# Performance work log

Hardware: AMD Instinct MI355X
Metric: run time of the kernel (lower is better)

## Reference

```python
import jax, jax.numpy as jnp
import numpy as np

B, E, DIM, RANK, K, P, H, W, FREQ = 16, 4, 64, 32, 2, 8, 128, 128, 64
NOISE_STD = 1.0 / E


def conv1x1(x, w):
    # x: [b,c,h,w], w: [o,c]
    return jnp.einsum('bchw,oc->bohw', x, w)


def dwconv(x, w, pad):
    # depthwise conv, w: [c,1,kh,kw]
    c = x.shape[1]
    return jax.lax.conv_general_dilated(
        x, w, (1, 1), [(pad, pad), (pad, pad)],
        dimension_numbers=('NCHW', 'OIHW', 'NCHW'), feature_group_count=c)


def patchify(x):
    b, c, h, w = x.shape
    return x.reshape(b, c, h // P, P, w // P, P).transpose(0, 1, 2, 4, 3, 5)


def unpatchify(x):
    b, c, hb, wb, p1, p2 = x.shape
    return x.transpose(0, 1, 2, 4, 3, 5).reshape(b, c, hb * p1, wb * p2)


def chan_layernorm(x, w, b):
    # WithBias LayerNorm over channel dim (to_3d puts c last)
    mu = x.mean(axis=1, keepdims=True)
    var = ((x - mu) ** 2).mean(axis=1, keepdims=True)
    return (x - mu) / jnp.sqrt(var + 1e-5) * w[None, :, None, None] + b[None, :, None, None]


def fft_attention(x, qw, qdw, kvw, kvdw, lnw, lnb, pow_, pob):
    q = dwconv(conv1x1(x, qw), qdw, 1)
    kv = dwconv(conv1x1(x, kvw), kvdw, 3)
    k, v = jnp.split(kv, 2, axis=1)
    qf = jnp.fft.rfft2(patchify(q))
    kf = jnp.fft.rfft2(patchify(k))
    out = jnp.fft.irfft2(qf * kf, s=(P, P))
    out = unpatchify(out)
    out = chan_layernorm(out, lnw, lnb)
    out = out * v
    return conv1x1(out, pow_) + pob[None, :, None, None]


def expert(p0, p1, p2, qw, qdw, kvw, kvdw, lnw, lnb, pow_, pob, x, shared):
    # ModExpert.process (feat_extract with depth>1 recomputes the same value)
    xr = conv1x1(x, p0)
    att = fft_attention(xr, qw, qdw, kvw, kvdw, lnw, lnb, pow_, pob)
    g = jax.nn.silu(conv1x1(shared, p1))
    return conv1x1(att * g, p2) + x


def setup_inputs() -> dict:
    key = jax.random.key(0)
    ks = jax.random.split(key, 20)
    s = 0.05
    return {
        'x': jax.random.normal(ks[0], (B, DIM, H, W), jnp.float32),
        'shared': jax.random.normal(ks[1], (B, DIM, H, W), jnp.float32),
        'freq_emb': jax.random.normal(ks[2], (B, FREQ), jnp.float32),
        'noise': jax.random.normal(ks[3], (B, E), jnp.float32),
        'gate_w': jax.random.normal(ks[4], (E, DIM), jnp.float32) * s,
        'freq_gate_w': jax.random.normal(ks[5], (E, FREQ), jnp.float32) * s,
        'p0': jax.random.normal(ks[6], (E, RANK, DIM), jnp.float32) * s,
        'p1': jax.random.normal(ks[7], (E, RANK, DIM), jnp.float32) * s,
        'p2': jax.random.normal(ks[8], (E, DIM, RANK), jnp.float32) * s,
        'q_w': jax.random.normal(ks[9], (E, RANK, RANK), jnp.float32) * s,
        'q_dw': jax.random.normal(ks[10], (E, RANK, 1, 3, 3), jnp.float32) * s,
        'kv_w': jax.random.normal(ks[11], (E, 2 * RANK, RANK), jnp.float32) * s,
        'kv_dw': jax.random.normal(ks[12], (E, 2 * RANK, 1, 7, 7), jnp.float32) * s,
        'ln_w': jnp.ones((E, RANK), jnp.float32),
        'ln_b': jnp.zeros((E, RANK), jnp.float32),
        'po_w': jax.random.normal(ks[13], (E, RANK, RANK), jnp.float32) * s,
        'po_b': jnp.zeros((E, RANK), jnp.float32),
    }


def reference(x, shared, freq_emb, noise, gate_w, freq_gate_w, p0, p1, p2,
              q_w, q_dw, kv_w, kv_dw, ln_w, ln_b, po_w, po_b):
    # RoutingFunction (eval mode: aux_loss = 0, noise still added)
    pooled = x.mean(axis=(2, 3))                       # [B, DIM]
    logits = pooled @ gate_w.T + freq_emb @ freq_gate_w.T  # [B, E]
    noisy = logits + noise * NOISE_STD
    scores = jax.nn.softmax(noisy, axis=-1)
    vals, idx = jax.lax.top_k(scores, K)
    gates = jnp.zeros_like(scores).at[jnp.arange(B)[:, None], idx].set(vals)
    # Dense expert evaluation; gated combine == SparseDispatcher dispatch/combine
    outs = jax.vmap(expert, in_axes=(0,) * 11 + (None, None))(
        p0, p1, p2, q_w, q_dw, kv_w, kv_dw, ln_w, ln_b, po_w, po_b, x, shared)
    return jnp.einsum('be,ebchw->bchw', gates, outs)
```

## Files before the change

### kernel.cpp

```cpp
#include <hip/hip_runtime.h>
#include <hip/hip_bf16.h>

#define BATCH 16
#define DIM 64
#define RANK 32
#define H 128
#define W 128
#define HW (H*W)
#define NSLOT 32

static __device__ __forceinline__ float bu2f(unsigned short u) {
    return __uint_as_float(((unsigned)u) << 16);
}
static __device__ __forceinline__ unsigned short f2bu(float f) {
    union { __hip_bfloat16 h; unsigned short u; } cv;
    cv.h = __float2bfloat16(f);
    return cv.u;
}
static __device__ __forceinline__ float ulo(unsigned int w) { return __uint_as_float(w << 16); }
static __device__ __forceinline__ float uhi(unsigned int w) { return __uint_as_float(w & 0xffff0000u); }

__global__ __launch_bounds__(256) void k_pool(const float* __restrict__ x,
                                              float* __restrict__ pooled) {
    int bc = blockIdx.x;
    const float4* p = (const float4*)(x + (size_t)bc * HW);
    float s = 0.f;
    for (int i = threadIdx.x; i < HW / 4; i += 256) {
        float4 v = p[i];
        s += v.x + v.y + v.z + v.w;
    }
#pragma unroll
    for (int off = 32; off > 0; off >>= 1) s += __shfl_down(s, off);
    __shared__ float red[4];
    if ((threadIdx.x & 63) == 0) red[threadIdx.x >> 6] = s;
    __syncthreads();
    if (threadIdx.x == 0)
        pooled[bc] = (red[0] + red[1] + red[2] + red[3]) * (1.f / HW);
}

__global__ __launch_bounds__(64) void k_gate(const float* __restrict__ pooled,
                                             const float* __restrict__ freq_emb,
                                             const float* __restrict__ noise,
                                             const float* __restrict__ gate_w,
                                             const float* __restrict__ fgw,
                                             int* __restrict__ slot_e,
                                             float* __restrict__ slot_g,
                                             float* __restrict__ gsum) {
    int b = threadIdx.x;
    if (b >= BATCH) return;
    float lg[4];
    for (int e = 0; e < 4; e++) {
        float s = 0.f;
        for (int c = 0; c < 64; c++) s += pooled[b * 64 + c] * gate_w[e * 64 + c];
        for (int c = 0; c < 64; c++) s += freq_emb[b * 64 + c] * fgw[e * 64 + c];
        s += noise[b * 4 + e] * 0.25f;
        lg[e] = s;
    }
    float m = fmaxf(fmaxf(lg[0], lg[1]), fmaxf(lg[2], lg[3]));
    float sc[4], Z = 0.f;
    for (int e = 0; e < 4; e++) { sc[e] = expf(lg[e] - m); Z += sc[e]; }
    for (int e = 0; e < 4; e++) sc[e] /= Z;
    int i0 = 0;
    for (int e = 1; e < 4; e++) if (sc[e] > sc[i0]) i0 = e;
    int i1 = -1;
    for (int e = 0; e < 4; e++) {
        if (e == i0) continue;
        if (i1 < 0 || sc[e] > sc[i1]) i1 = e;
    }
    slot_e[2 * b] = i0;     slot_g[2 * b] = sc[i0];
    slot_e[2 * b + 1] = i1; slot_g[2 * b + 1] = sc[i1];
    gsum[b] = sc[i0] + sc[i1];
}

__global__ __launch_bounds__(256) void k_weff(const float* __restrict__ q_w,
                                              const float* __restrict__ kv_w,
                                              const float* __restrict__ p0,
                                              float* __restrict__ weff) {
    int t = blockIdx.x * 256 + threadIdx.x;
    if (t >= 4 * 96 * 64) return;
    int c = t & 63;
    int j = (t >> 6) % 96;
    int e = t / (96 * 64);
    const float* p0p = p0 + (size_t)e * RANK * DIM;
    float s = 0.f;
    if (j < 32) {
        const float* qp = q_w + (e * 32 + j) * 32;
        for (int r = 0; r < 32; r++) s += qp[r] * p0p[r * DIM + c];
    } else {
        const float* kp = kv_w + (e * 64 + (j - 32)) * 32;
        for (int r = 0; r < 32; r++) s += kp[r] * p0p[r * DIM + c];
    }
    weff[(e * 64 + c) * 96 + j] = s;
}

__global__ __launch_bounds__(256) void k_xpose(const float* __restrict__ po_w,
                                               const float* __restrict__ p1,
                                               float* __restrict__ powf,
                                               float* __restrict__ p1f) {
    int t = blockIdx.x * 256 + threadIdx.x;
    if (t < 4096) {
        int e = t >> 10, oc = (t >> 5) & 31, c = t & 31;
        powf[(e * 32 + c) * 32 + oc] = po_w[t];
    }
    int e = t >> 11, j = (t >> 6) & 31, c = t & 63;
    p1f[(e * 64 + c) * 32 + j] = p1[t];
}

__global__ __launch_bounds__(256) void k_qkvpre(const float* __restrict__ x,
                                                const float* __restrict__ weff,
                                                const int* __restrict__ slot_e,
                                                unsigned short* __restrict__ qkvpre) {
    int t = blockIdx.x;
    int jg = t % 3;
    int tile = (t / 3) & 15;
    int slot = t / 48;
    int b = slot >> 1;
    int e = slot_e[slot];
    const float* wp = weff + e * 96 * 64 + jg * 32;
    int p0 = tile * 1024 + threadIdx.x * 4;
    const float* xb = x + (size_t)b * DIM * HW + p0;
    float a0[32], a1[32], a2[32], a3[32];
#pragma unroll
    for (int j = 0; j < 32; j++) { a0[j] = 0.f; a1[j] = 0.f; a2[j] = 0.f; a3[j] = 0.f; }
    for (int c = 0; c < DIM; c++) {
        float4 xv = *(const float4*)(xb + (size_t)c * HW);
        const float* wr = wp + c * 96;
#pragma unroll
        for (int j = 0; j < 32; j++) {
            float wv = wr[j];
            a0[j] += wv * xv.x; a1[j] += wv * xv.y; a2[j] += wv * xv.z; a3[j] += wv * xv.w;
        }
    }
    unsigned short* op = qkvpre + ((size_t)slot * 96 + jg * 32) * HW + p0;
#pragma unroll
    for (int j = 0; j < 32; j++) {
        ushort4 o4;
        o4.x = f2bu(a0[j]); o4.y = f2bu(a1[j]); o4.z = f2bu(a2[j]); o4.w = f2bu(a3[j]);
        *(ushort4*)(op + (size_t)j * HW) = o4;
    }
}

__global__ __launch_bounds__(256) void k_dw(const unsigned short* __restrict__ qkvpre,
                                            const float* __restrict__ q_dw,
                                            const float* __restrict__ kv_dw,
                                            const int* __restrict__ slot_e,
                                            unsigned short* __restrict__ qkv) {
    __shared__ unsigned short S[38][144];
    int t = blockIdx.x;
    int tile = t & 3;
    int c = (t >> 2) % 96;
    int slot = t / (96 * 4);
    int e = slot_e[slot];
    const unsigned short* in = qkvpre + ((size_t)slot * 96 + c) * HW;
    int y0 = tile * 32 - 3;

    float wk[49];
    if (c < 32) {
        const float* wp = q_dw + (e * 32 + c) * 9;
#pragma unroll
        for (int i = 0; i < 9; i++) wk[i] = wp[i];
    } else {
        const float* wp = kv_dw + (e * 64 + (c - 32)) * 49;
#pragma unroll
        for (int i = 0; i < 49; i++) wk[i] = wp[i];
    }

    for (int i = threadIdx.x; i < 38 * 16; i += 256) {
        int r = i >> 4;
        int xc = (i & 15) << 3;
        int yy = y0 + r;
        uint4 v = make_uint4(0u, 0u, 0u, 0u);
        if (yy >= 0 && yy < H) v = *(const uint4*)(in + (size_t)yy * W + xc);
        *(uint4*)&S[r][8 + xc] = v;
    }
    for (int i = threadIdx.x; i < 38 * 2; i += 256) {
        int r = i >> 1;
        *(uint4*)&S[r][(i & 1) ? 136 : 0] = make_uint4(0u, 0u, 0u, 0u);
    }
    __syncthreads();

    int tx = (threadIdx.x & 31) * 4;
    int ty0 = (threadIdx.x >> 5) * 4;
    float acc[4][4];
#pragma unroll
    for (int a_ = 0; a_ < 4; a_++)
#pragma unroll
        for (int b_ = 0; b_ < 4; b_++) acc[a_][b_] = 0.f;

    if (c < 32) {
#pragma unroll
        for (int rr = 0; rr < 6; rr++) {
            int srow = ty0 + 2 + rr;
            float px[12];
            uint2 w0 = *(const uint2*)&S[srow][4 + tx];
            uint2 w1 = *(const uint2*)&S[srow][8 + tx];
            uint2 w2 = *(const uint2*)&S[srow][12 + tx];
            px[0] = ulo(w0.x); px[1] = uhi(w0.x); px[2] = ulo(w0.y); px[3] = uhi(w0.y);
            px[4] = ulo(w1.x); px[5] = uhi(w1.x); px[6] = ulo(w1.y); px[7] = uhi(w1.y);
            px[8] = ulo(w2.x); px[9] = uhi(w2.x); px[10] = ulo(w2.y); px[11] = uhi(w2.y);
#pragma unroll
            for (int ly = 0; ly < 4; ly++) {
                int ky = rr - ly;
                if (ky < 0 || ky > 2) continue;
#pragma unroll
                for (int kx = 0; kx < 3; kx++) {
                    float wv = wk[ky * 3 + kx];
#pragma unroll
                    for (int j = 0; j < 4; j++) acc[ly][j] += wv * px[j + kx + 3];
                }
            }
        }
    } else {
#pragma unroll
        for (int rr = 0; rr < 10; rr++) {
            int srow = ty0 + rr;
            float px[12];
            uint2 w0 = *(const uint2*)&S[srow][4 + tx];
            uint2 w1 = *(const uint2*)&S[srow][8 + tx];
            uint2 w2 = *(const uint2*)&S[srow][12 + tx];
            px[0] = ulo(w0.x); px[1] = uhi(w0.x); px[2] = ulo(w0.y); px[3] = uhi(w0.y);
            px[4] = ulo(w1.x); px[5] = uhi(w1.x); px[6] = ulo(w1.y); px[7] = uhi(w1.y);
            px[8] = ulo(w2.x); px[9] = uhi(w2.x); px[10] = ulo(w2.y); px[11] = uhi(w2.y);
#pragma unroll
            for (int ly = 0; ly < 4; ly++) {
                int ky = rr - ly;
                if (ky < 0 || ky > 6) continue;
#pragma unroll
                for (int kx = 0; kx < 7; kx++) {
                    float wv = wk[ky * 7 + kx];
#pragma unroll
                    for (int j = 0; j < 4; j++) acc[ly][j] += wv * px[j + kx + 1];
                }
            }
        }
    }

    unsigned short* op = qkv + ((size_t)slot * 96 + c) * HW;
    int ybase = tile * 32 + ty0;
#pragma unroll
    for (int ly = 0; ly < 4; ly++) {
        ushort4 o4;
        o4.x = f2bu(acc[ly][0]); o4.y = f2bu(acc[ly][1]);
        o4.z = f2bu(acc[ly][2]); o4.w = f2bu(acc[ly][3]);
        *(ushort4*)(op + (size_t)(ybase + ly) * W + tx) = o4;
    }
}

__global__ __launch_bounds__(256) void k_circ(const unsigned short* __restrict__ qkv,
                                              unsigned short* __restrict__ obuf) {
    __shared__ float Qs[32][68];
    __shared__ float Kp[32][68];
    int u = threadIdx.x >> 3;
    int i = threadIdx.x & 7;
    int U = blockIdx.x * 32 + u;
    int patch = U & 255;
    int c = (U >> 8) & 31;
    int slot = U >> 13;
    int py = patch >> 4, px = patch & 15;
    size_t rowbase = ((size_t)slot * 96 + c) * HW + (py * 8 + i) * W + px * 8;
    uint4 qu = *(const uint4*)(qkv + rowbase);
    uint4 ku = *(const uint4*)(qkv + rowbase + (size_t)32 * HW);
    float qr[8], kr[8];
    qr[0] = ulo(qu.x); qr[1] = uhi(qu.x); qr[2] = ulo(qu.y); qr[3] = uhi(qu.y);
    qr[4] = ulo(qu.z); qr[5] = uhi(qu.z); qr[6] = ulo(qu.w); qr[7] = uhi(qu.w);
    kr[0] = ulo(ku.x); kr[1] = uhi(ku.x); kr[2] = ulo(ku.y); kr[3] = uhi(ku.y);
    kr[4] = ulo(ku.z); kr[5] = uhi(ku.z); kr[6] = ulo(ku.w); kr[7] = uhi(ku.w);
    *(float4*)&Qs[u][i * 8] = *(float4*)&qr[0];
    *(float4*)&Qs[u][i * 8 + 4] = *(float4*)&qr[4];
    *(float4*)&Kp[u][i * 8] = *(float4*)&kr[0];
    *(float4*)&Kp[u][i * 8 + 4] = *(float4*)&kr[4];
    __syncthreads();
    float acc[8];
#pragma unroll
    for (int j = 0; j < 8; j++) acc[j] = 0.f;
#pragma unroll
    for (int mi = 0; mi < 8; mi++) {
        int r = (i - mi) & 7;
        float qv[8], ka[4], kb[4];
        *(float4*)&qv[0] = *(const float4*)&Qs[u][mi * 8];
        *(float4*)&qv[4] = *(const float4*)&Qs[u][mi * 8 + 4];
        *(float4*)&ka[0] = *(const float4*)&Kp[u][r * 8];
        *(float4*)&kb[0] = *(const float4*)&Kp[u][r * 8 + 4];
#pragma unroll
        for (int j = 0; j < 8; j++) {
            float s = acc[j];
#pragma unroll
            for (int t = 0; t < 4; t++) {
                s += ka[t] * qv[(j - t) & 7];
                s += kb[t] * qv[(j - 4 - t) & 7];
            }
            acc[j] = s;
        }
    }
    size_t obase = ((size_t)slot * 32 + c) * HW + (py * 8 + i) * W + px * 8;
    uint4 ov;
    ov.x = (unsigned)f2bu(acc[0]) | ((unsigned)f2bu(acc[1]) << 16);
    ov.y = (unsigned)f2bu(acc[2]) | ((unsigned)f2bu(acc[3]) << 16);
    ov.z = (unsigned)f2bu(acc[4]) | ((unsigned)f2bu(acc[5]) << 16);
    ov.w = (unsigned)f2bu(acc[6]) | ((unsigned)f2bu(acc[7]) << 16);
    *(uint4*)(obuf + obase) = ov;
}

__global__ __launch_bounds__(256) void k_att(const unsigned short* __restrict__ obuf,
                                             const unsigned short* __restrict__ qkv,
                                             const float* __restrict__ shr,
                                             const int* __restrict__ slot_e,
                                             const float* __restrict__ slot_g,
                                             const float* __restrict__ powf,
                                             const float* __restrict__ po_b,
                                             const float* __restrict__ ln_w,
                                             const float* __restrict__ ln_b,
                                             const float* __restrict__ p1f,
                                             unsigned short* __restrict__ attg) {
    int slot = blockIdx.x >> 6;
    int p = ((blockIdx.x & 63) << 8) + threadIdx.x;
    int b = slot >> 1;
    int e = slot_e[slot];
    float g = slot_g[slot];

    const unsigned short* op = obuf + (size_t)slot * 32 * HW + p;
    float o[32];
#pragma unroll
    for (int c = 0; c < 32; c++) o[c] = bu2f(op[(size_t)c * HW]);
    float mu = 0.f;
#pragma unroll
    for (int c = 0; c < 32; c++) mu += o[c];
    mu *= (1.f / 32.f);
    float var = 0.f;
#pragma unroll
    for (int c = 0; c < 32; c++) { float d = o[c] - mu; var += d * d; }
    float rinv = rsqrtf(var * (1.f / 32.f) + 1e-5f);
    const float* powp = powf + e * 1024;
    const float* lnwp = ln_w + e * 32;
    const float* lnbp = ln_b + e * 32;
    const float* pobp = po_b + e * 32;
    const unsigned short* vp = qkv + ((size_t)slot * 96 + 64) * HW + p;
    float att[32];
#pragma unroll
    for (int j = 0; j < 32; j++) att[j] = pobp[j];
    for (int c = 0; c < 32; c++) {
        float uu = ((o[c] - mu) * rinv * lnwp[c] + lnbp[c]) * bu2f(vp[(size_t)c * HW]);
        const float* pr = powp + c * 32;
#pragma unroll
        for (int j = 0; j < 32; j++) att[j] += pr[j] * uu;
    }

    float t[32];
#pragma unroll
    for (int j = 0; j < 32; j++) t[j] = 0.f;
    const float* shp = shr + (size_t)b * 64 * HW + p;
    const float* p1p = p1f + e * 2048;
    for (int c = 0; c < 64; c++) {
        float sv = shp[(size_t)c * HW];
        const float* pr = p1p + c * 32;
#pragma unroll
        for (int j = 0; j < 32; j++) t[j] += pr[j] * sv;
    }

    unsigned short* ap = attg + ((size_t)slot * HW + p) * 32;
    unsigned int wbuf[16];
#pragma unroll
    for (int jj = 0; jj < 16; jj++) {
        float t0 = t[2 * jj], t1 = t[2 * jj + 1];
        float a0 = g * att[2 * jj] * t0 * __builtin_amdgcn_rcpf(1.f + __expf(-t0));
        float a1 = g * att[2 * jj + 1] * t1 * __builtin_amdgcn_rcpf(1.f + __expf(-t1));
        wbuf[jj] = (unsigned)f2bu(a0) | ((unsigned)f2bu(a1) << 16);
    }
#pragma unroll
    for (int q = 0; q < 4; q++)
        *(uint4*)(ap + q * 8) = *(uint4*)&wbuf[q * 4];
}

__global__ __launch_bounds__(256) void k_comb(const unsigned short* __restrict__ attg,
                                              const float* __restrict__ x,
                                              const int* __restrict__ slot_e,
                                              const float* __restrict__ gsum,
                                              const float* __restrict__ p2,
                                              float* __restrict__ out) {
    int t = blockIdx.x;
    int oh = t & 1;
    int tile = (t >> 1) & 63;
    int b = t >> 7;
    int p = (tile << 8) + threadIdx.x;

    const unsigned short* a0p = attg + ((size_t)(2 * b) * HW + p) * 32;
    const unsigned short* a1p = attg + ((size_t)(2 * b + 1) * HW + p) * 32;
    float a0[32], a1[32];
#pragma unroll
    for (int q = 0; q < 4; q++) {
        uint4 u0 = *(const uint4*)(a0p + q * 8);
        uint4 u1 = *(const uint4*)(a1p + q * 8);
        a0[q * 8 + 0] = ulo(u0.x); a0[q * 8 + 1] = uhi(u0.x);
        a0[q * 8 + 2] = ulo(u0.y); a0[q * 8 + 3] = uhi(u0.y);
        a0[q * 8 + 4] = ulo(u0.z); a0[q * 8 + 5] = uhi(u0.z);
        a0[q * 8 + 6] = ulo(u0.w); a0[q * 8 + 7] = uhi(u0.w);
        a1[q * 8 + 0] = ulo(u1.x); a1[q * 8 + 1] = uhi(u1.x);
        a1[q * 8 + 2] = ulo(u1.y); a1[q * 8 + 3] = uhi(u1.y);
        a1[q * 8 + 4] = ulo(u1.z); a1[q * 8 + 5] = uhi(u1.z);
        a1[q * 8 + 6] = ulo(u1.w); a1[q * 8 + 7] = uhi(u1.w);
    }
    int e0 = slot_e[2 * b], e1 = slot_e[2 * b + 1];
    float gs = gsum[b];
    const float* p2a = p2 + e0 * 2048 + oh * 1024;
    const float* p2b = p2 + e1 * 2048 + oh * 1024;
    const float* xp = x + ((size_t)b * 64 + oh * 32) * HW + p;
    float* oa = out + ((size_t)b * 64 + oh * 32) * HW + p;
    for (int oc = 0; oc < 32; oc++) {
        const float* pa = p2a + oc * 32;
        const float* pb = p2b + oc * 32;
        float sa = 0.f, sb = 0.f;
#pragma unroll
        for (int j = 0; j < 32; j++) {
            sa += pa[j] * a0[j];
            sb += pb[j] * a1[j];
        }
        oa[(size_t)oc * HW] = sa + sb + gs * xp[(size_t)oc * HW];
    }
}

extern "C" void kernel_launch(void* const* d_in, const int* in_sizes, int n_in,
                              void* d_out, int out_size, void* d_ws, size_t ws_size,
                              hipStream_t stream) {
    (void)in_sizes; (void)n_in; (void)out_size; (void)ws_size;
    const float* x      = (const float*)d_in[0];
    const float* shr    = (const float*)d_in[1];
    const float* femb   = (const float*)d_in[2];
    const float* noise  = (const float*)d_in[3];
    const float* gate_w = (const float*)d_in[4];
    const float* fgw    = (const float*)d_in[5];
    const float* p0     = (const float*)d_in[6];
    const float* p1     = (const float*)d_in[7];
    const float* p2     = (const float*)d_in[8];
    const float* q_w    = (const float*)d_in[9];
    const float* q_dw   = (const float*)d_in[10];
    const float* kv_w   = (const float*)d_in[11];
    const float* kv_dw  = (const float*)d_in[12];
    const float* ln_w   = (const float*)d_in[13];
    const float* ln_b   = (const float*)d_in[14];
    const float* po_w   = (const float*)d_in[15];
    const float* po_b   = (const float*)d_in[16];
    float* out = (float*)d_out;

    float* fws = (float*)d_ws;
    float* pooled = fws; fws += 1024;
    float* gsum   = fws; fws += 16;
    float* slot_g = fws; fws += 32;
    int*   slot_e = (int*)fws; fws += 32;
    float* weff   = fws; fws += 4 * 96 * 64;
    float* powf   = fws; fws += 4096;
    float* p1f    = fws; fws += 8192;
    uintptr_t a = ((uintptr_t)fws + 255) & ~(uintptr_t)255;
    unsigned short* qkvpre = (unsigned short*)a;
    unsigned short* qkvb   = qkvpre + (size_t)NSLOT * 96 * HW;
    unsigned short* obuf   = qkvb + (size_t)NSLOT * 96 * HW;
    unsigned short* attg   = qkvpre;

    k_pool<<<1024, 256, 0, stream>>>(x, pooled);
    k_gate<<<1, 64, 0, stream>>>(pooled, femb, noise, gate_w, fgw, slot_e, slot_g, gsum);
    k_weff<<<96, 256, 0, stream>>>(q_w, kv_w, p0, weff);
    k_xpose<<<32, 256, 0, stream>>>(po_w, p1, powf, p1f);
    k_qkvpre<<<NSLOT * 48, 256, 0, stream>>>(x, weff, slot_e, qkvpre);
    k_dw<<<NSLOT * 96 * 4, 256, 0, stream>>>(qkvpre, q_dw, kv_dw, slot_e, qkvb);
    k_circ<<<NSLOT * 32 * 256 / 32, 256, 0, stream>>>(qkvb, obuf);
    k_att<<<NSLOT * 64, 256, 0, stream>>>(obuf, qkvb, shr, slot_e, slot_g,
                                          powf, po_b, ln_w, ln_b, p1f, attg);
    k_comb<<<BATCH * 128, 256, 0, stream>>>(attg, x, slot_e, gsum, p2, out);
}
```

Baseline: 487.3 us.

## Compute qkv pre-projection with split-bf16 MFMA instead of scalar FMAs

The 1x1 projection in k_qkvpre moves from per-thread scalar FP32 FMA loops to bf16 MFMA 16x16x32 instructions. Both the weights and the input activations are split into high and low bf16 parts, and three MFMAs per tile approximate an FP32 product. Input pixels are transposed into swizzled LDS tiles, and weights are stored as pre-split bf16 in an [e][j][c] layout. This removes the scalar FP32 compute bottleneck at the cost of extra split arithmetic, LDS staging, and scattered 2-byte output stores.

```diff
diff --git a/kernel.cpp b/kernel.cpp
--- a/kernel.cpp
+++ b/kernel.cpp
@@ -8,6 +8,9 @@
 #define W 128
 #define HW (H*W)
 #define NSLOT 32
+
+typedef __attribute__((ext_vector_type(8))) short short8;
+typedef __attribute__((ext_vector_type(4))) float f32x4;
 
 static __device__ __forceinline__ float bu2f(unsigned short u) {
     return __uint_as_float(((unsigned)u) << 16);
@@ -75,7 +78,8 @@
 __global__ __launch_bounds__(256) void k_weff(const float* __restrict__ q_w,
                                               const float* __restrict__ kv_w,
                                               const float* __restrict__ p0,
-                                              float* __restrict__ weff) {
+                                              unsigned short* __restrict__ weff_h,
+                                              unsigned short* __restrict__ weff_l) {
     int t = blockIdx.x * 256 + threadIdx.x;
     if (t >= 4 * 96 * 64) return;
     int c = t & 63;
@@ -90,7 +94,10 @@
         const float* kp = kv_w + (e * 64 + (j - 32)) * 32;
         for (int r = 0; r < 32; r++) s += kp[r] * p0p[r * DIM + c];
     }
-    weff[(e * 64 + c) * 96 + j] = s;
+    int idx = (e * 96 + j) * 64 + c;
+    unsigned short hv = f2bu(s);
+    weff_h[idx] = hv;
+    weff_l[idx] = f2bu(s - bu2f(hv));
 }
 
 __global__ __launch_bounds__(256) void k_xpose(const float* __restrict__ po_w,
@@ -107,36 +114,88 @@
 }
 
 __global__ __launch_bounds__(256) void k_qkvpre(const float* __restrict__ x,
-                                                const float* __restrict__ weff,
+                                                const unsigned short* __restrict__ weff_h,
+                                                const unsigned short* __restrict__ weff_l,
                                                 const int* __restrict__ slot_e,
                                                 unsigned short* __restrict__ qkvpre) {
-    int t = blockIdx.x;
-    int jg = t % 3;
-    int tile = (t / 3) & 15;
-    int slot = t / 48;
+    __shared__ __align__(16) unsigned short XT[2][128 * 64];
+    int blk = blockIdx.x;
+    int slot = blk >> 7;
+    int p0 = (blk & 127) << 7;
     int b = slot >> 1;
     int e = slot_e[slot];
-    const float* wp = weff + e * 96 * 64 + jg * 32;
-    int p0 = tile * 1024 + threadIdx.x * 4;
-    const float* xb = x + (size_t)b * DIM * HW + p0;
-    float a0[32], a1[32], a2[32], a3[32];
-#pragma unroll
-    for (int j = 0; j < 32; j++) { a0[j] = 0.f; a1[j] = 0.f; a2[j] = 0.f; a3[j] = 0.f; }
-    for (int c = 0; c < DIM; c++) {
-        float4 xv = *(const float4*)(xb + (size_t)c * HW);
-        const float* wr = wp + c * 96;
-#pragma unroll
-        for (int j = 0; j < 32; j++) {
-            float wv = wr[j];
-            a0[j] += wv * xv.x; a1[j] += wv * xv.y; a2[j] += wv * xv.z; a3[j] += wv * xv.w;
-        }
-    }
-    unsigned short* op = qkvpre + ((size_t)slot * 96 + jg * 32) * HW + p0;
-#pragma unroll
-    for (int j = 0; j < 32; j++) {
-        ushort4 o4;
-        o4.x = f2bu(a0[j]); o4.y = f2bu(a1[j]); o4.z = f2bu(a2[j]); o4.w = f2bu(a3[j]);
-        *(ushort4*)(op + (size_t)j * HW) = o4;
+
+    {
+        int t = threadIdx.x;
+        int px = t & 127;
+        int ch = (t >> 7) << 5;
+        const float* xb = x + ((size_t)b * 64 + ch) * HW + p0 + px;
+        unsigned short hv[32] __attribute__((aligned(16)));
+        unsigned short lv[32] __attribute__((aligned(16)));
+#pragma unroll
+        for (int c = 0; c < 32; c++) {
+            float v = xb[(size_t)c * HW];
+            unsigned short h = f2bu(v);
+            hv[c] = h;
+            lv[c] = f2bu(v - bu2f(h));
+        }
+        int rowbyte = px * 128;
+        int sw = (px & 7) << 4;
+#pragma unroll
+        for (int k = 0; k < 4; k++) {
+            int byt = (rowbyte + (ch + k * 8) * 2) ^ sw;
+            *(uint4*)((char*)XT[0] + byt) = *(const uint4*)&hv[k * 8];
+            *(uint4*)((char*)XT[1] + byt) = *(const uint4*)&lv[k * 8];
+        }
+    }
+    __syncthreads();
+
+    int w = threadIdx.x >> 6;
+    int l = threadIdx.x & 63;
+    int li = l & 15, lq = l >> 4;
+
+    short8 Bf[2][2][2];
+#pragma unroll
+    for (int nt = 0; nt < 2; nt++) {
+        int pxl = (w << 5) + (nt << 4) + li;
+        int sw = (pxl & 7) << 4;
+#pragma unroll
+        for (int kt = 0; kt < 2; kt++) {
+            int byt = (pxl * 128 + kt * 64 + lq * 16) ^ sw;
+            Bf[nt][kt][0] = *(const short8*)((char*)XT[0] + byt);
+            Bf[nt][kt][1] = *(const short8*)((char*)XT[1] + byt);
+        }
+    }
+
+    const unsigned short* wh = weff_h + ((size_t)e * 96 + li) * 64 + lq * 8;
+    const unsigned short* wl = weff_l + ((size_t)e * 96 + li) * 64 + lq * 8;
+
+#pragma unroll
+    for (int mt = 0; mt < 6; mt++) {
+        short8 Ah[2], Al[2];
+#pragma unroll
+        for (int kt = 0; kt < 2; kt++) {
+            Ah[kt] = *(const short8*)(wh + (mt * 16) * 64 + kt * 32);
+            Al[kt] = *(const short8*)(wl + (mt * 16) * 64 + kt * 32);
+        }
+        f32x4 acc[2] = {{0.f, 0.f, 0.f, 0.f}, {0.f, 0.f, 0.f, 0.f}};
+#pragma unroll
+        for (int nt = 0; nt < 2; nt++) {
+#pragma unroll
+            for (int kt = 0; kt < 2; kt++) {
+                acc[nt] = __builtin_amdgcn_mfma_f32_16x16x32_bf16(Ah[kt], Bf[nt][kt][0], acc[nt], 0, 0, 0);
+                acc[nt] = __builtin_amdgcn_mfma_f32_16x16x32_bf16(Ah[kt], Bf[nt][kt][1], acc[nt], 0, 0, 0);
+                acc[nt] = __builtin_amdgcn_mfma_f32_16x16x32_bf16(Al[kt], Bf[nt][kt][0], acc[nt], 0, 0, 0);
+            }
+        }
+#pragma unroll
+        for (int nt = 0; nt < 2; nt++) {
+            int p = p0 + (w << 5) + (nt << 4) + li;
+            unsigned short* op = qkvpre + ((size_t)slot * 96 + mt * 16 + lq * 4) * HW + p;
+#pragma unroll
+            for (int r = 0; r < 4; r++)
+                op[(size_t)r * HW] = f2bu(acc[nt][r]);
+        }
     }
 }
 
@@ -446,7 +505,8 @@
     float* gsum   = fws; fws += 16;
     float* slot_g = fws; fws += 32;
     int*   slot_e = (int*)fws; fws += 32;
-    float* weff   = fws; fws += 4 * 96 * 64;
+    unsigned short* weffh = (unsigned short*)fws; fws += 12288;
+    unsigned short* weffl = (unsigned short*)fws; fws += 12288;
     float* powf   = fws; fws += 4096;
     float* p1f    = fws; fws += 8192;
     uintptr_t a = ((uintptr_t)fws + 255) & ~(uintptr_t)255;
@@ -457,9 +517,9 @@
 
     k_pool<<<1024, 256, 0, stream>>>(x, pooled);
     k_gate<<<1, 64, 0, stream>>>(pooled, femb, noise, gate_w, fgw, slot_e, slot_g, gsum);
-    k_weff<<<96, 256, 0, stream>>>(q_w, kv_w, p0, weff);
+    k_weff<<<96, 256, 0, stream>>>(q_w, kv_w, p0, weffh, weffl);
     k_xpose<<<32, 256, 0, stream>>>(po_w, p1, powf, p1f);
-    k_qkvpre<<<NSLOT * 48, 256, 0, stream>>>(x, weff, slot_e, qkvpre);
+    k_qkvpre<<<NSLOT * 128, 256, 0, stream>>>(x, weffh, weffl, slot_e, qkvpre);
     k_dw<<<NSLOT * 96 * 4, 256, 0, stream>>>(qkvpre, q_dw, kv_dw, slot_e, qkvb);
     k_circ<<<NSLOT * 32 * 256 / 32, 256, 0, stream>>>(qkvb, obuf);
     k_att<<<NSLOT * 64, 256, 0, stream>>>(obuf, qkvb, shr, slot_e, slot_g,
```

Measured after the change: 469.1 us. 3.7% less time.
